# Kernel optimization log

Measured on AMD Instinct MI355X. Metric: run time of the kernel, lower is better.

The kernel has to match this reference:

```python
import jax, jax.numpy as jnp
import numpy as np

B, S, D, H, L, DFF = 32, 512, 1024, 16, 4, 2048
DK = D // H
NEG = -1e32
EPS = 1e-5


def setup_inputs() -> dict:
    key = jax.random.key(0)
    ks = jax.random.split(key, 8)
    std = 0.02
    inp = {
        "q_embed": jax.random.normal(ks[0], (B, S, D), jnp.float32),
        "qa_embed": jax.random.normal(ks[1], (B, S, D), jnp.float32),
        # per-block stacked params [L, ...]; torch Linear stored as [in, out]
        "Wk": jax.random.normal(ks[2], (L, D, D), jnp.float32) * std,
        "bk": jnp.zeros((L, D), jnp.float32),
        "Wv": jax.random.normal(ks[3], (L, D, D), jnp.float32) * std,
        "bv": jnp.zeros((L, D), jnp.float32),
        "Wo": jax.random.normal(ks[4], (L, D, D), jnp.float32) * std,
        "bo": jnp.zeros((L, D), jnp.float32),
        "ln1_s": jnp.ones((L, D), jnp.float32),
        "ln1_b": jnp.zeros((L, D), jnp.float32),
        "W1": jax.random.normal(ks[5], (L, D, DFF), jnp.float32) * std,
        "b1": jnp.zeros((L, DFF), jnp.float32),
        "W2": jax.random.normal(ks[6], (L, DFF, D), jnp.float32) * std,
        "b2": jnp.zeros((L, D), jnp.float32),
        "ln2_s": jnp.ones((L, D), jnp.float32),
        "ln2_b": jnp.zeros((L, D), jnp.float32),
    }
    return inp


def _ln(x, s, b):
    m = jnp.mean(x, axis=-1, keepdims=True)
    v = jnp.mean((x - m) ** 2, axis=-1, keepdims=True)
    return (x - m) / jnp.sqrt(v + EPS) * s + b


def _block(x, y, Wk, bk, Wv, bv, Wo, bo, l1s, l1b, W1, b1, W2, b2, l2s, l2b, allowed):
    # kq_same=1: q and k both use k_linear; q == k since query == key == x
    qk = (x @ Wk + bk).reshape(B, S, H, DK).transpose(0, 2, 1, 3)  # [B,H,S,DK]
    v = (y @ Wv + bv).reshape(B, S, H, DK).transpose(0, 2, 1, 3)
    scores = jnp.einsum("bhid,bhjd->bhij", qk, qk) / np.sqrt(DK)
    scores = jnp.where(allowed, scores, NEG)  # strictly-causal mask
    attn = jax.nn.softmax(scores, axis=-1)
    attn = attn * (jnp.arange(S)[None, None, :, None] > 0)  # zero_pad row 0
    o = jnp.einsum("bhij,bhjd->bhid", attn, v)  # [B,H,S,DK]
    o = o.transpose(0, 2, 1, 3).reshape(B, S, D) @ Wo + bo
    x = _ln(x + o, l1s, l1b)
    f = jax.nn.relu(x @ W1 + b1) @ W2 + b2
    return _ln(x + f, l2s, l2b)


def reference(q_embed, qa_embed, Wk, bk, Wv, bv, Wo, bo, ln1_s, ln1_b,
              W1, b1, W2, b2, ln2_s, ln2_b):
    allowed = jnp.tril(jnp.ones((S, S), bool), -1)  # j < i
    x, y = q_embed, qa_embed
    for i in range(L):
        x = _block(x, y, Wk[i], bk[i], Wv[i], bv[i], Wo[i], bo[i],
                   ln1_s[i], ln1_b[i], W1[i], b1[i], W2[i], b2[i],
                   ln2_s[i], ln2_b[i], allowed)
    return x
```

## Files before the change

kernel.cpp:

```cpp
#include <hip/hip_runtime.h>

#define B_ 32
#define S_ 512
#define D_ 1024
#define H_ 16
#define DK_ 64
#define DFF_ 2048
#define L_ 4

typedef __attribute__((ext_vector_type(8))) short short8;
typedef __attribute__((ext_vector_type(4))) float f32x4;
typedef unsigned short u16;
typedef unsigned int u32;
typedef __attribute__((ext_vector_type(4))) u16 u16x4;
typedef __attribute__((ext_vector_type(8))) u16 u16x8;

__device__ __forceinline__ u16 f2bf(float f) {
    u32 u = __float_as_uint(f);
    u = u + 0x7fffu + ((u >> 16) & 1u);
    return (u16)(u >> 16);
}
__device__ __forceinline__ u16 f2bf_t(float f) {
    return (u16)(__float_as_uint(f) >> 16);
}
__device__ __forceinline__ float bf2f(u16 v) {
    return __uint_as_float(((u32)v) << 16);
}

__device__ __forceinline__ void async16(const u16* g, u16* l) {
    __builtin_amdgcn_global_load_lds((const __attribute__((address_space(1))) u32*)g,
                                     (__attribute__((address_space(3))) u32*)l, 16, 0, 0);
}

#define READ_A(P)                                                              \
    afr[0][0] = *(const short8*)&lds[cb + arow + (2*(P)+0)*1024 + chv0];       \
    afr[0][1] = *(const short8*)&lds[cb + arow + (2*(P)+0)*1024 + chv1];       \
    afr[1][0] = *(const short8*)&lds[cb + arow + (2*(P)+1)*1024 + chv0];       \
    afr[1][1] = *(const short8*)&lds[cb + arow + (2*(P)+1)*1024 + chv1];

#define MFMA_PHASE(P)                                                          \
    __builtin_amdgcn_s_barrier();                                              \
    asm volatile("s_waitcnt lgkmcnt(0)" ::: "memory");                         \
    __builtin_amdgcn_sched_barrier(0);                                         \
    __builtin_amdgcn_s_setprio(1);                                             \
    _Pragma("unroll")                                                          \
    for (int mi2 = 0; mi2 < 2; mi2++) {                                        \
        _Pragma("unroll")                                                      \
        for (int ni = 0; ni < 4; ni++) {                                       \
            acc[2*(P)+mi2][ni] = __builtin_amdgcn_mfma_f32_16x16x32_bf16(      \
                afr[mi2][0], bfr[ni][0], acc[2*(P)+mi2][ni], 0, 0, 0);         \
            acc[2*(P)+mi2][ni] = __builtin_amdgcn_mfma_f32_16x16x32_bf16(      \
                afr[mi2][1], bfr[ni][1], acc[2*(P)+mi2][ni], 0, 0, 0);         \
        }                                                                      \
    }                                                                          \
    __builtin_amdgcn_s_setprio(0);

template<int RELU, int OUTM>
__global__ __launch_bounds__(512, 2)
void gemm256(const u16* __restrict__ A, const u16* __restrict__ Bt,
             const float* __restrict__ bias, void* __restrict__ C,
             int M, int N, int K)
{
    __shared__ __align__(16) u16 lds[65536];
    const int t = threadIdx.x;
    const int w = t >> 6, l = t & 63;
    const int lane16 = l & 15, quad = l >> 4;
    const int wm = w >> 2, wn = w & 3;

    const int gx = gridDim.x;
    const int nwg = gx * gridDim.y;
    const int orig = blockIdx.y * gx + blockIdx.x;
    const int q8 = nwg >> 3, r8 = nwg & 7;
    const int xcd = orig & 7, sidx = orig >> 3;
    const int nid = (xcd < r8 ? xcd * (q8 + 1) : r8 * (q8 + 1) + (xcd - r8) * q8) + sidx;
    const int m0 = (nid / gx) * 256;
    const int n0 = (nid % gx) * 256;

    f32x4 acc[8][4];
#pragma unroll
    for (int i = 0; i < 8; i++)
#pragma unroll
        for (int j = 0; j < 4; j++) acc[i][j] = f32x4{0.f, 0.f, 0.f, 0.f};

    const int lr = l >> 3;
    const int xorcol = ((l & 7) ^ lr) * 8;
    const int aw8 = (w < 4 ? w * 8 : 128 + (w - 4) * 8);
    const u16* Asrc = A + (size_t)(m0 + aw8 + lr) * K + xorcol;
    const u16* Bsrc = Bt + (size_t)(n0 + w * 8 + lr) * K + xorcol;

    auto stageA = [&](int tile, int q) {
        const int c = tile & 1;
        async16(Asrc + (size_t)(q * 32) * K + (tile << 6),
                &lds[c * 16384 + (aw8 + q * 32) * 64]);
    };
    auto stageB = [&](int tile, int j) {
        const int c = tile & 1;
        async16(Bsrc + (size_t)(j * 64) * K + (tile << 6),
                &lds[32768 + c * 16384 + (j * 64 + w * 8) * 64]);
    };

    const int chv0 = ((0 + quad) ^ (lane16 & 7)) * 8;
    const int chv1 = ((4 + quad) ^ (lane16 & 7)) * 8;
    const int arow = (wm * 128 + lane16) * 64;
    const int brow = 32768 + (wn * 64 + lane16) * 64;

    const int NT = K >> 6;

    stageA(0, 0); stageB(0, 0); stageB(0, 1);
    stageA(0, 1); stageB(0, 2); stageB(0, 3);
    stageA(0, 2);
    stageA(0, 3);
    stageA(1, 0); stageB(1, 0); stageB(1, 1);
    stageA(1, 1); stageB(1, 2); stageB(1, 3);
    stageA(1, 2);
    asm volatile("s_waitcnt vmcnt(7)" ::: "memory");
    __builtin_amdgcn_sched_barrier(0);
    __builtin_amdgcn_s_barrier();

    for (int tt = 0; tt < NT; tt++) {
        const int cb = (tt & 1) * 16384;
        short8 bfr[4][2], afr[2][2];
        if (tt + 1 < NT) stageA(tt + 1, 3);
#pragma unroll
        for (int ni = 0; ni < 4; ni++) {
            bfr[ni][0] = *(const short8*)&lds[cb + brow + ni * 1024 + chv0];
            bfr[ni][1] = *(const short8*)&lds[cb + brow + ni * 1024 + chv1];
        }
        READ_A(0)
        MFMA_PHASE(0)
        __builtin_amdgcn_s_barrier();
        if (tt + 2 < NT) { stageA(tt + 2, 0); stageB(tt + 2, 0); stageB(tt + 2, 1); }
        READ_A(1)
        MFMA_PHASE(1)
        __builtin_amdgcn_s_barrier();
        if (tt + 2 < NT) { stageA(tt + 2, 1); stageB(tt + 2, 2); stageB(tt + 2, 3); }
        READ_A(2)
        MFMA_PHASE(2)
        __builtin_amdgcn_s_barrier();
        if (tt + 2 < NT) stageA(tt + 2, 2);
        READ_A(3)
        MFMA_PHASE(3)
        if (tt + 2 < NT) asm volatile("s_waitcnt vmcnt(7)" ::: "memory");
        else             asm volatile("s_waitcnt vmcnt(0)" ::: "memory");
        __builtin_amdgcn_sched_barrier(0);
        __builtin_amdgcn_s_barrier();
    }

#pragma unroll
    for (int mi = 0; mi < 8; mi++) {
#pragma unroll
        for (int ni = 0; ni < 4; ni++) {
            int col = n0 + wn * 64 + ni * 16 + lane16;
            float bv = bias[col];
            if (OUTM == 2) {
                int tok0 = m0 + wm * 128 + mi * 16 + quad * 4;
                int bb = tok0 >> 9, s0 = tok0 & 511;
                int hh = col >> 6, dd = col & 63;
                u16x4 pk;
#pragma unroll
                for (int r2 = 0; r2 < 4; r2++) pk[r2] = f2bf(acc[mi][ni][r2] + bv);
                *(u16x4*)&((u16*)C)[(((size_t)bb * H_ + hh) * DK_ + dd) * S_ + s0] = pk;
            } else {
                int row = m0 + wm * 128 + mi * 16 + quad * 4;
#pragma unroll
                for (int r2 = 0; r2 < 4; r2++) {
                    float v = acc[mi][ni][r2] + bv;
                    if (RELU) v = fmaxf(v, 0.f);
                    size_t idx = (size_t)(row + r2) * N + col;
                    if (OUTM == 1) ((u16*)C)[idx] = f2bf(v);
                    else           ((float*)C)[idx] = v;
                }
            }
        }
    }
}

__global__ __launch_bounds__(256, 3)
void attn_kernel(const u16* __restrict__ qk, const u16* __restrict__ vt,
                 u16* __restrict__ ao)
{
    __shared__ __align__(16) u16 sP[4][32 * 72];
    const int t = threadIdx.x, w = t >> 6, l = t & 63;
    const int lane16 = l & 15, quad = l >> 4;
    const int p = blockIdx.x;
    const int bh = blockIdx.y;
    const int b = bh >> 4, h = bh & 15;
    const int band = (w < 2) ? (2 * p + w) : (15 - 2 * p - (w - 2));
    const int band0 = band * 32;
    const u16* kb = qk + (size_t)b * S_ * D_ + h * DK_;
    const u16* vb = vt + (size_t)bh * DK_ * S_;
    u16* aob = ao + (size_t)b * S_ * D_ + h * DK_;
    const float SC = 0.125f * 1.44269504f;
    u16* myP = sP[w];

    short8 bq[2][2];
#pragma unroll
    for (int ii = 0; ii < 2; ii++)
#pragma unroll
        for (int kf = 0; kf < 2; kf++)
            bq[ii][kf] = *(const short8*)(kb + (size_t)(band0 + ii * 16 + lane16) * D_ +
                                          kf * 32 + quad * 8);

    f32x4 aco[4][2];
    float lsum[2] = {0.f, 0.f};
#pragma unroll
    for (int di = 0; di < 4; di++)
#pragma unroll
        for (int ii = 0; ii < 2; ii++) aco[di][ii] = f32x4{0.f, 0.f, 0.f, 0.f};

    const int ntiles = (band >> 1) + 1;
    for (int jt = 0; jt < ntiles; jt++) {
        const int j0 = jt * 64;
        const bool diag = (jt == ntiles - 1);

        short8 aK[2][4];
#pragma unroll
        for (int kf = 0; kf < 2; kf++)
#pragma unroll
            for (int ji = 0; ji < 4; ji++)
                aK[kf][ji] = *(const short8*)(kb + (size_t)(j0 + ji * 16 + lane16) * D_ +
                                              kf * 32 + quad * 8);
        f32x4 sacc[4][2];
#pragma unroll
        for (int ji = 0; ji < 4; ji++)
#pragma unroll
            for (int ii = 0; ii < 2; ii++) sacc[ji][ii] = f32x4{0.f, 0.f, 0.f, 0.f};
#pragma unroll
        for (int kf = 0; kf < 2; kf++)
#pragma unroll
            for (int ji = 0; ji < 4; ji++)
#pragma unroll
                for (int ii = 0; ii < 2; ii++)
                    sacc[ji][ii] = __builtin_amdgcn_mfma_f32_16x16x32_bf16(
                        aK[kf][ji], bq[ii][kf], sacc[ji][ii], 0, 0, 0);

        short8 aV[2][4];
#pragma unroll
        for (int kf = 0; kf < 2; kf++)
#pragma unroll
            for (int di = 0; di < 4; di++)
                aV[kf][di] = *(const short8*)(vb + (size_t)(di * 16 + lane16) * S_ +
                                              j0 + kf * 32 + quad * 8);

#pragma unroll
        for (int ii = 0; ii < 2; ii++) {
#pragma unroll
            for (int ji = 0; ji < 4; ji++) {
                u16x4 pk;
#pragma unroll
                for (int r2 = 0; r2 < 4; r2++) {
                    float v = sacc[ji][ii][r2] * SC;
                    if (diag) {
                        int j = j0 + ji * 16 + quad * 4 + r2;
                        int i = band0 + ii * 16 + lane16;
                        if (j >= i) v = -3e38f;
                    }
                    float pv = exp2f(v);
                    lsum[ii] += pv;
                    pk[r2] = f2bf_t(pv);
                }
                *(u16x4*)&myP[(ii * 16 + lane16) * 72 + ji * 16 + quad * 4] = pk;
            }
        }

        short8 pf[2][2];
#pragma unroll
        for (int kf = 0; kf < 2; kf++)
#pragma unroll
            for (int ii = 0; ii < 2; ii++)
                pf[kf][ii] = *(const short8*)&myP[(ii * 16 + lane16) * 72 +
                                                  kf * 32 + quad * 8];
#pragma unroll
        for (int kf = 0; kf < 2; kf++)
#pragma unroll
            for (int di = 0; di < 4; di++)
#pragma unroll
                for (int ii = 0; ii < 2; ii++)
                    aco[di][ii] = __builtin_amdgcn_mfma_f32_16x16x32_bf16(
                        aV[kf][di], pf[kf][ii], aco[di][ii], 0, 0, 0);
    }

#pragma unroll
    for (int ii = 0; ii < 2; ii++) {
        lsum[ii] += __shfl_xor(lsum[ii], 16);
        lsum[ii] += __shfl_xor(lsum[ii], 32);
    }

#pragma unroll
    for (int ii = 0; ii < 2; ii++) {
        int row = band0 + ii * 16 + lane16;
        float lv = lsum[ii];
        float inv = (row == 0 || !(lv > 0.f)) ? 0.f : 1.f / lv;
#pragma unroll
        for (int di = 0; di < 4; di++) {
            u16x4 o;
#pragma unroll
            for (int r2 = 0; r2 < 4; r2++) o[r2] = f2bf(aco[di][ii][r2] * inv);
            *(u16x4*)&aob[(size_t)row * D_ + di * 16 + quad * 4] = o;
        }
    }
}

template<int XBF, int WF32>
__global__ __launch_bounds__(256)
void ln_kernel(const void* __restrict__ xin, const float* __restrict__ addv,
               const float* __restrict__ sc, const float* __restrict__ bi,
               u16* __restrict__ xb_out, float* __restrict__ f32_out)
{
    const int row = blockIdx.x;
    const int t = threadIdx.x;
    const int w = t >> 6, l = t & 63;
    __shared__ float red[8];
    f32x4 a;
    if (XBF) {
        u16x4 raw = ((const u16x4*)xin)[(size_t)row * 256 + t];
#pragma unroll
        for (int j = 0; j < 4; j++) a[j] = bf2f(raw[j]);
    } else {
        a = ((const f32x4*)xin)[(size_t)row * 256 + t];
    }
    f32x4 c = ((const f32x4*)(addv + (size_t)row * D_))[t];
    f32x4 v;
    float s1 = 0.f, s2 = 0.f;
#pragma unroll
    for (int j = 0; j < 4; j++) {
        v[j] = a[j] + c[j];
        s1 += v[j];
        s2 += v[j] * v[j];
    }
#pragma unroll
    for (int off = 32; off > 0; off >>= 1) {
        s1 += __shfl_xor(s1, off);
        s2 += __shfl_xor(s2, off);
    }
    if (l == 0) { red[w * 2] = s1; red[w * 2 + 1] = s2; }
    __syncthreads();
    s1 = red[0] + red[2] + red[4] + red[6];
    s2 = red[1] + red[3] + red[5] + red[7];
    float mean = s1 * (1.f / D_);
    float var = s2 * (1.f / D_) - mean * mean;
    float rstd = rsqrtf(var + 1e-5f);
    f32x4 s4 = ((const f32x4*)sc)[t];
    f32x4 b4 = ((const f32x4*)bi)[t];
    f32x4 o;
    u16x4 ob;
#pragma unroll
    for (int j = 0; j < 4; j++) {
        o[j] = (v[j] - mean) * rstd * s4[j] + b4[j];
        ob[j] = f2bf(o[j]);
    }
    ((u16x4*)(xb_out + (size_t)row * D_))[t] = ob;
    if (WF32) ((f32x4*)(f32_out + (size_t)row * D_))[t] = o;
}

__global__ void cvt_kernel(const float* __restrict__ in, u16* __restrict__ out, int n4)
{
    int i = blockIdx.x * blockDim.x + threadIdx.x;
    if (i < n4) {
        f32x4 v = ((const f32x4*)in)[i];
        u16x4 o;
#pragma unroll
        for (int j = 0; j < 4; j++) o[j] = f2bf(v[j]);
        ((u16x4*)out)[i] = o;
    }
}

__device__ __forceinline__ void tconv_body(const float* W, u16* WT, int K, int N,
                                           int bx, int by, int t)
{
    __shared__ float tile[64][65];
    const int n0 = bx * 64, k0 = by * 64;
#pragma unroll
    for (int i = 0; i < 4; i++) {
        int kr = (t >> 4) + i * 16;
        int nc = (t & 15) * 4;
        f32x4 v = *(const f32x4*)&W[(size_t)(k0 + kr) * N + n0 + nc];
        tile[kr][nc] = v[0]; tile[kr][nc + 1] = v[1];
        tile[kr][nc + 2] = v[2]; tile[kr][nc + 3] = v[3];
    }
    __syncthreads();
#pragma unroll
    for (int i = 0; i < 4; i++) {
        int nr = (t >> 4) + i * 16;
        int kc = (t & 15) * 4;
        u16x4 o;
#pragma unroll
        for (int j = 0; j < 4; j++) o[j] = f2bf(tile[kc + j][nr]);
        *(u16x4*)&WT[(size_t)(n0 + nr) * K + k0 + kc] = o;
    }
}

__global__ __launch_bounds__(256)
void wconv_kernel(const float* __restrict__ Wk, const float* __restrict__ Wv,
                  const float* __restrict__ Wo, const float* __restrict__ W1f,
                  const float* __restrict__ W2f,
                  u16* __restrict__ wk, u16* __restrict__ wv, u16* __restrict__ wo,
                  u16* __restrict__ w1, u16* __restrict__ w2)
{
    const int idx = blockIdx.x;
    const float* W; u16* T; int K, N, bx, by;
    if (idx < 768) {
        int wsel = idx >> 8, t16 = idx & 255;
        W = (wsel == 0) ? Wk : (wsel == 1) ? Wv : Wo;
        T = (wsel == 0) ? wk : (wsel == 1) ? wv : wo;
        K = 1024; N = 1024; bx = t16 & 15; by = t16 >> 4;
    } else if (idx < 1280) {
        int i = idx - 768;
        W = W1f; T = w1; K = 1024; N = 2048; bx = i & 31; by = i >> 5;
    } else {
        int i = idx - 1280;
        W = W2f; T = w2; K = 2048; N = 1024; bx = i & 15; by = i >> 4;
    }
    tconv_body(W, T, K, N, bx, by, threadIdx.x);
}

extern "C" void kernel_launch(void* const* d_in, const int* in_sizes, int n_in,
                              void* d_out, int out_size, void* d_ws, size_t ws_size,
                              hipStream_t stream)
{
    const float* q_embed = (const float*)d_in[0];
    const float* qa_embed = (const float*)d_in[1];
    const float* Wk = (const float*)d_in[2];
    const float* bk = (const float*)d_in[3];
    const float* Wv = (const float*)d_in[4];
    const float* bv = (const float*)d_in[5];
    const float* Wo = (const float*)d_in[6];
    const float* bo = (const float*)d_in[7];
    const float* ln1_s = (const float*)d_in[8];
    const float* ln1_b = (const float*)d_in[9];
    const float* W1 = (const float*)d_in[10];
    const float* b1 = (const float*)d_in[11];
    const float* W2 = (const float*)d_in[12];
    const float* b2 = (const float*)d_in[13];
    const float* ln2_s = (const float*)d_in[14];
    const float* ln2_b = (const float*)d_in[15];
    (void)in_sizes; (void)n_in; (void)out_size;

    char* ws = (char*)d_ws;
    size_t off = 0;
    auto carve = [&](size_t bytes) -> char* {
        char* p = ws + off;
        off += (bytes + 255) & ~(size_t)255;
        return p;
    };
    const size_t NTOK = (size_t)B_ * S_;
    u16* wk = (u16*)carve((size_t)D_ * D_ * 2);
    u16* wv = (u16*)carve((size_t)D_ * D_ * 2);
    u16* wo = (u16*)carve((size_t)D_ * D_ * 2);
    u16* w1 = (u16*)carve((size_t)D_ * DFF_ * 2);
    u16* w2 = (u16*)carve((size_t)DFF_ * D_ * 2);
    u16* x = (u16*)carve(NTOK * D_ * 2);
    u16* U12 = (u16*)carve(NTOK * DFF_ * 2);
    u16* U3 = (u16*)carve(NTOK * D_ * 2);
    size_t off_overlay = off;
    u16* ybf_sep = (u16*)carve(NTOK * D_ * 2);
    bool sep = (ws_size >= off);
    if (!sep) off = off_overlay;
    if (ws_size < off) return;

    u16* qkb = U12;
    u16* vbf = U12 + NTOK * D_;
    u16* hb = U12;
    u16* aob = U3;
    u16* ybf = sep ? ybf_sep : U3;
    float* of32 = (float*)d_out;

    cvt_kernel<<<16384, 256, 0, stream>>>(q_embed, x, (int)(NTOK * D_ / 4));
    if (sep)
        cvt_kernel<<<16384, 256, 0, stream>>>(qa_embed, ybf, (int)(NTOK * D_ / 4));

    const dim3 G1024(4, 64), G2048(8, 64);
    for (int lyr = 0; lyr < L_; lyr++) {
        const size_t wsq = (size_t)lyr * D_ * D_;
        const size_t wf1 = (size_t)lyr * D_ * DFF_;
        wconv_kernel<<<1792, 256, 0, stream>>>(Wk + wsq, Wv + wsq, Wo + wsq,
                                               W1 + wf1, W2 + wf1,
                                               wk, wv, wo, w1, w2);
        if (!sep)
            cvt_kernel<<<16384, 256, 0, stream>>>(qa_embed, ybf, (int)(NTOK * D_ / 4));
        gemm256<0, 1><<<G1024, 512, 0, stream>>>(x, wk, bk + lyr * D_,
                                                 qkb, (int)NTOK, D_, D_);
        gemm256<0, 2><<<G1024, 512, 0, stream>>>(ybf, wv, bv + lyr * D_,
                                                 vbf, (int)NTOK, D_, D_);
        attn_kernel<<<dim3(4, B_ * H_), 256, 0, stream>>>(qkb, vbf, aob);
        gemm256<0, 0><<<G1024, 512, 0, stream>>>(aob, wo, bo + lyr * D_,
                                                 of32, (int)NTOK, D_, D_);
        if (lyr == 0)
            ln_kernel<0, 0><<<(int)NTOK, 256, 0, stream>>>(q_embed, of32,
                ln1_s + lyr * D_, ln1_b + lyr * D_, x, nullptr);
        else
            ln_kernel<1, 0><<<(int)NTOK, 256, 0, stream>>>(x, of32,
                ln1_s + lyr * D_, ln1_b + lyr * D_, x, nullptr);
        gemm256<1, 1><<<G2048, 512, 0, stream>>>(x, w1, b1 + lyr * DFF_,
                                                 hb, (int)NTOK, DFF_, D_);
        gemm256<0, 0><<<G1024, 512, 0, stream>>>(hb, w2, b2 + lyr * D_,
                                                 of32, (int)NTOK, D_, DFF_);
        if (lyr == L_ - 1)
            ln_kernel<1, 1><<<(int)NTOK, 256, 0, stream>>>(x, of32,
                ln2_s + lyr * D_, ln2_b + lyr * D_, x, (float*)d_out);
        else
            ln_kernel<1, 0><<<(int)NTOK, 256, 0, stream>>>(x, of32,
                ln2_s + lyr * D_, ln2_b + lyr * D_, x, nullptr);
    }
}
```

Baseline: 1.798 ms.

## Software-pipeline LDS fragment reads against MFMAs in GEMM main loop

Restructures the GEMM K-loop into eight MFMA phases, each split by k-half. The A/B fragment reads for the next phase are issued from LDS while the current phase's MFMAs run, with partial lgkmcnt waits instead of full drains. The next tile's first fragments are prefetched across the iteration boundary, and the global-to-LDS staging order is rebalanced to interleave A and B loads. The aim is to hide LDS latency behind MFMA work. In exchange there are more barriers per tile and more register pressure, and the hand-tuned waitcnt counts must match the exact read order to stay correct.

```diff
diff --git a/kernel.cpp b/kernel.cpp
--- a/kernel.cpp
+++ b/kernel.cpp
@@ -32,28 +32,29 @@
                                      (__attribute__((address_space(3))) u32*)l, 16, 0, 0);
 }
 
-#define READ_A(P)                                                              \
-    afr[0][0] = *(const short8*)&lds[cb + arow + (2*(P)+0)*1024 + chv0];       \
-    afr[0][1] = *(const short8*)&lds[cb + arow + (2*(P)+0)*1024 + chv1];       \
-    afr[1][0] = *(const short8*)&lds[cb + arow + (2*(P)+1)*1024 + chv0];       \
-    afr[1][1] = *(const short8*)&lds[cb + arow + (2*(P)+1)*1024 + chv1];
-
-#define MFMA_PHASE(P)                                                          \
-    __builtin_amdgcn_s_barrier();                                              \
-    asm volatile("s_waitcnt lgkmcnt(0)" ::: "memory");                         \
+#define RD_A2(dst, CBX, MP, CHV)                                               \
+    dst[0] = *(const short8*)&lds[(CBX) + arow + (2*(MP)+0)*1024 + (CHV)];     \
+    dst[1] = *(const short8*)&lds[(CBX) + arow + (2*(MP)+1)*1024 + (CHV)];
+
+#define RD_B4(dst, CBX, CHV)                                                   \
+    _Pragma("unroll")                                                          \
+    for (int ni = 0; ni < 4; ni++)                                             \
+        dst[ni] = *(const short8*)&lds[32768 + (CBX) + browr + ni*1024 + (CHV)];
+
+#define MF8(MP, ASRC, BSRC, LGN)                                               \
+    asm volatile("s_waitcnt lgkmcnt(" #LGN ")" ::: "memory");                  \
     __builtin_amdgcn_sched_barrier(0);                                         \
     __builtin_amdgcn_s_setprio(1);                                             \
     _Pragma("unroll")                                                          \
-    for (int mi2 = 0; mi2 < 2; mi2++) {                                        \
-        _Pragma("unroll")                                                      \
-        for (int ni = 0; ni < 4; ni++) {                                       \
-            acc[2*(P)+mi2][ni] = __builtin_amdgcn_mfma_f32_16x16x32_bf16(      \
-                afr[mi2][0], bfr[ni][0], acc[2*(P)+mi2][ni], 0, 0, 0);         \
-            acc[2*(P)+mi2][ni] = __builtin_amdgcn_mfma_f32_16x16x32_bf16(      \
-                afr[mi2][1], bfr[ni][1], acc[2*(P)+mi2][ni], 0, 0, 0);         \
-        }                                                                      \
+    for (int ni = 0; ni < 4; ni++) {                                           \
+        acc[2*(MP)+0][ni] = __builtin_amdgcn_mfma_f32_16x16x32_bf16(           \
+            ASRC[0], BSRC[ni], acc[2*(MP)+0][ni], 0, 0, 0);                    \
+        acc[2*(MP)+1][ni] = __builtin_amdgcn_mfma_f32_16x16x32_bf16(           \
+            ASRC[1], BSRC[ni], acc[2*(MP)+1][ni], 0, 0, 0);                    \
     }                                                                          \
-    __builtin_amdgcn_s_setprio(0);
+    __builtin_amdgcn_s_setprio(0);                                             \
+    __builtin_amdgcn_s_barrier();                                              \
+    __builtin_amdgcn_sched_barrier(0);
 
 template<int RELU, int OUTM>
 __global__ __launch_bounds__(512, 2)
@@ -101,49 +102,63 @@
 
     const int chv0 = ((0 + quad) ^ (lane16 & 7)) * 8;
     const int chv1 = ((4 + quad) ^ (lane16 & 7)) * 8;
-    const int arow = (wm * 128 + lane16) * 64;
-    const int brow = 32768 + (wn * 64 + lane16) * 64;
+    const int arow  = (wm * 128 + lane16) * 64;
+    const int browr = (wn * 64 + lane16) * 64;
 
     const int NT = K >> 6;
 
-    stageA(0, 0); stageB(0, 0); stageB(0, 1);
-    stageA(0, 1); stageB(0, 2); stageB(0, 3);
-    stageA(0, 2);
-    stageA(0, 3);
-    stageA(1, 0); stageB(1, 0); stageB(1, 1);
-    stageA(1, 1); stageB(1, 2); stageB(1, 3);
-    stageA(1, 2);
-    asm volatile("s_waitcnt vmcnt(7)" ::: "memory");
+    stageA(0, 0); stageB(0, 0); stageA(0, 1); stageB(0, 1);
+    stageA(0, 2); stageB(0, 2); stageA(0, 3); stageB(0, 3);
+    stageA(1, 0); stageB(1, 0); stageA(1, 1); stageB(1, 1);
+    stageA(1, 2); stageB(1, 2);
+    asm volatile("s_waitcnt vmcnt(6)" ::: "memory");
     __builtin_amdgcn_sched_barrier(0);
     __builtin_amdgcn_s_barrier();
 
+    short8 a0[2], a1[2], bk0[4], bk1[4];
+    RD_B4(bk0, 0, chv0)
+    RD_A2(a0, 0, 0, chv0)
+
     for (int tt = 0; tt < NT; tt++) {
-        const int cb = (tt & 1) * 16384;
-        short8 bfr[4][2], afr[2][2];
-        if (tt + 1 < NT) stageA(tt + 1, 3);
-#pragma unroll
-        for (int ni = 0; ni < 4; ni++) {
-            bfr[ni][0] = *(const short8*)&lds[cb + brow + ni * 1024 + chv0];
-            bfr[ni][1] = *(const short8*)&lds[cb + brow + ni * 1024 + chv1];
-        }
-        READ_A(0)
-        MFMA_PHASE(0)
-        __builtin_amdgcn_s_barrier();
-        if (tt + 2 < NT) { stageA(tt + 2, 0); stageB(tt + 2, 0); stageB(tt + 2, 1); }
-        READ_A(1)
-        MFMA_PHASE(1)
-        __builtin_amdgcn_s_barrier();
-        if (tt + 2 < NT) { stageA(tt + 2, 1); stageB(tt + 2, 2); stageB(tt + 2, 3); }
-        READ_A(2)
-        MFMA_PHASE(2)
-        __builtin_amdgcn_s_barrier();
-        if (tt + 2 < NT) stageA(tt + 2, 2);
-        READ_A(3)
-        MFMA_PHASE(3)
-        if (tt + 2 < NT) asm volatile("s_waitcnt vmcnt(7)" ::: "memory");
-        else             asm volatile("s_waitcnt vmcnt(0)" ::: "memory");
+        const int cb  = (tt & 1) << 14;
+        const int cbn = ((tt + 1) & 1) << 14;
+        const bool hn1 = (tt + 1 < NT);
+        const bool hn2 = (tt + 2 < NT);
+
+        RD_A2(a1, cb, 1, chv0)
+        MF8(0, a0, bk0, 2)
+        if (hn1) { stageA(tt + 1, 3); stageB(tt + 1, 3); }
+        RD_A2(a0, cb, 2, chv0)
+        bk1[0] = *(const short8*)&lds[32768 + cb + browr + 0 * 1024 + chv1];
+        bk1[1] = *(const short8*)&lds[32768 + cb + browr + 1 * 1024 + chv1];
+        MF8(1, a1, bk0, 4)
+        RD_A2(a1, cb, 3, chv0)
+        bk1[2] = *(const short8*)&lds[32768 + cb + browr + 2 * 1024 + chv1];
+        bk1[3] = *(const short8*)&lds[32768 + cb + browr + 3 * 1024 + chv1];
+        MF8(2, a0, bk0, 6)
+        RD_A2(a0, cb, 0, chv1)
+        MF8(3, a1, bk0, 4)
+        RD_A2(a1, cb, 1, chv1)
+        MF8(0, a0, bk1, 2)
+        if (hn2) { stageA(tt + 2, 0); stageB(tt + 2, 0); }
+        RD_A2(a0, cb, 2, chv1)
+        MF8(1, a1, bk1, 2)
+        if (hn2) { stageA(tt + 2, 1); stageB(tt + 2, 1); }
+        RD_A2(a1, cb, 3, chv1)
+        MF8(2, a0, bk1, 2)
+        if (hn2) { stageA(tt + 2, 2); stageB(tt + 2, 2); }
+        if (hn2) asm volatile("s_waitcnt vmcnt(6)" ::: "memory");
+        else     asm volatile("s_waitcnt vmcnt(0)" ::: "memory");
         __builtin_amdgcn_sched_barrier(0);
         __builtin_amdgcn_s_barrier();
+        __builtin_amdgcn_sched_barrier(0);
+        if (hn1) {
+            RD_B4(bk0, cbn, chv0)
+            RD_A2(a0, cbn, 0, chv0)
+            MF8(3, a1, bk1, 6)
+        } else {
+            MF8(3, a1, bk1, 0)
+        }
     }
 
 #pragma unroll
```

New measurement: 1.793 ms. About the same (-0.3%).

## Restructure GEMM main loop into quadrant MFMA phases with 2x unrolled double-buffer

Applied to the files above, without the earlier changes.

Replaces the four row-phase MFMA schedule with a quadrant schedule: each wave loads a 4-row A quarter and a 2-column B half, so fragments are reused across two MFMA quadrants. The loop is unrolled by two K tiles so buffer offsets are compile-time constants. Global-to-LDS staging is interleaved between the quadrant phases with explicit barriers and waitcnts. The goal is to reduce LDS read traffic per MFMA and overlap loads with compute better. The cost is more barriers per tile and a tighter dependency on exact waitcnt counts.

```diff
diff --git a/kernel.cpp b/kernel.cpp
--- a/kernel.cpp
+++ b/kernel.cpp
@@ -32,28 +32,38 @@
                                      (__attribute__((address_space(3))) u32*)l, 16, 0, 0);
 }
 
-#define READ_A(P)                                                              \
-    afr[0][0] = *(const short8*)&lds[cb + arow + (2*(P)+0)*1024 + chv0];       \
-    afr[0][1] = *(const short8*)&lds[cb + arow + (2*(P)+0)*1024 + chv1];       \
-    afr[1][0] = *(const short8*)&lds[cb + arow + (2*(P)+1)*1024 + chv0];       \
-    afr[1][1] = *(const short8*)&lds[cb + arow + (2*(P)+1)*1024 + chv1];
-
-#define MFMA_PHASE(P)                                                          \
-    __builtin_amdgcn_s_barrier();                                              \
+#define LGKM0_FENCE                                                            \
     asm volatile("s_waitcnt lgkmcnt(0)" ::: "memory");                         \
-    __builtin_amdgcn_sched_barrier(0);                                         \
+    __builtin_amdgcn_sched_barrier(0);
+
+#define MFQ(MQ, NQ, BQ)                                                        \
     __builtin_amdgcn_s_setprio(1);                                             \
     _Pragma("unroll")                                                          \
-    for (int mi2 = 0; mi2 < 2; mi2++) {                                        \
+    for (int r = 0; r < 4; r++) {                                              \
         _Pragma("unroll")                                                      \
-        for (int ni = 0; ni < 4; ni++) {                                       \
-            acc[2*(P)+mi2][ni] = __builtin_amdgcn_mfma_f32_16x16x32_bf16(      \
-                afr[mi2][0], bfr[ni][0], acc[2*(P)+mi2][ni], 0, 0, 0);         \
-            acc[2*(P)+mi2][ni] = __builtin_amdgcn_mfma_f32_16x16x32_bf16(      \
-                afr[mi2][1], bfr[ni][1], acc[2*(P)+mi2][ni], 0, 0, 0);         \
+        for (int c = 0; c < 2; c++) {                                          \
+            _Pragma("unroll")                                                  \
+            for (int kf = 0; kf < 2; kf++)                                     \
+                acc[(MQ)*4+r][(NQ)*2+c] =                                      \
+                    __builtin_amdgcn_mfma_f32_16x16x32_bf16(                   \
+                        a[r][kf], BQ[c][kf], acc[(MQ)*4+r][(NQ)*2+c], 0,0,0);  \
         }                                                                      \
     }                                                                          \
     __builtin_amdgcn_s_setprio(0);
+
+#define RD_AQ(CBA, MQ)                                                         \
+    _Pragma("unroll")                                                          \
+    for (int r = 0; r < 4; r++) {                                              \
+        a[r][0] = *(const short8*)&lds[(CBA) + arow + (MQ)*4096 + r*1024 + chv0]; \
+        a[r][1] = *(const short8*)&lds[(CBA) + arow + (MQ)*4096 + r*1024 + chv1]; \
+    }
+
+#define RD_BQ(DST, CBB, NQ)                                                    \
+    _Pragma("unroll")                                                          \
+    for (int c = 0; c < 2; c++) {                                              \
+        DST[c][0] = *(const short8*)&lds[(CBB) + brow + (NQ)*2048 + c*1024 + chv0]; \
+        DST[c][1] = *(const short8*)&lds[(CBB) + brow + (NQ)*2048 + c*1024 + chv1]; \
+    }
 
 template<int RELU, int OUTM>
 __global__ __launch_bounds__(512, 2)
@@ -102,46 +112,76 @@
     const int chv0 = ((0 + quad) ^ (lane16 & 7)) * 8;
     const int chv1 = ((4 + quad) ^ (lane16 & 7)) * 8;
     const int arow = (wm * 128 + lane16) * 64;
-    const int brow = 32768 + (wn * 64 + lane16) * 64;
+    const int brow = (wn * 64 + lane16) * 64;
 
     const int NT = K >> 6;
-
-    stageA(0, 0); stageB(0, 0); stageB(0, 1);
-    stageA(0, 1); stageB(0, 2); stageB(0, 3);
-    stageA(0, 2);
-    stageA(0, 3);
-    stageA(1, 0); stageB(1, 0); stageB(1, 1);
-    stageA(1, 1); stageB(1, 2); stageB(1, 3);
-    stageA(1, 2);
-    asm volatile("s_waitcnt vmcnt(7)" ::: "memory");
+    const int niter = NT >> 1;
+
+    stageA(0, 0); stageA(0, 1); stageA(0, 2); stageA(0, 3);
+    stageB(0, 0); stageB(0, 1); stageB(0, 2); stageB(0, 3);
+    stageA(1, 0); stageA(1, 1);
+    stageB(1, 0); stageB(1, 1); stageB(1, 2); stageB(1, 3);
+    stageA(1, 2); stageA(1, 3);
+    asm volatile("s_waitcnt vmcnt(8)" ::: "memory");
     __builtin_amdgcn_sched_barrier(0);
     __builtin_amdgcn_s_barrier();
 
-    for (int tt = 0; tt < NT; tt++) {
-        const int cb = (tt & 1) * 16384;
-        short8 bfr[4][2], afr[2][2];
-        if (tt + 1 < NT) stageA(tt + 1, 3);
-#pragma unroll
-        for (int ni = 0; ni < 4; ni++) {
-            bfr[ni][0] = *(const short8*)&lds[cb + brow + ni * 1024 + chv0];
-            bfr[ni][1] = *(const short8*)&lds[cb + brow + ni * 1024 + chv1];
-        }
-        READ_A(0)
-        MFMA_PHASE(0)
-        __builtin_amdgcn_s_barrier();
-        if (tt + 2 < NT) { stageA(tt + 2, 0); stageB(tt + 2, 0); stageB(tt + 2, 1); }
-        READ_A(1)
-        MFMA_PHASE(1)
-        __builtin_amdgcn_s_barrier();
-        if (tt + 2 < NT) { stageA(tt + 2, 1); stageB(tt + 2, 2); stageB(tt + 2, 3); }
-        READ_A(2)
-        MFMA_PHASE(2)
-        __builtin_amdgcn_s_barrier();
-        if (tt + 2 < NT) stageA(tt + 2, 2);
-        READ_A(3)
-        MFMA_PHASE(3)
-        if (tt + 2 < NT) asm volatile("s_waitcnt vmcnt(7)" ::: "memory");
-        else             asm volatile("s_waitcnt vmcnt(0)" ::: "memory");
+    short8 a[4][2], b0[2][2], b1[2][2];
+
+    for (int it = 0; it < niter; it++) {
+        const bool hn = (it + 1 < niter);
+        const int e2 = 2 * it + 2, o2 = 2 * it + 3;
+
+        RD_AQ(0, 0)
+        RD_BQ(b0, 32768, 0)
+        asm volatile("s_waitcnt lgkmcnt(8)" ::: "memory");
+        __builtin_amdgcn_s_barrier();
+        LGKM0_FENCE
+        MFQ(0, 0, b0)
+        __builtin_amdgcn_s_barrier();
+        RD_BQ(b1, 32768, 1)
+        if (hn) { stageA(e2, 0); stageA(e2, 1); }
+        __builtin_amdgcn_s_barrier();
+        LGKM0_FENCE
+        MFQ(0, 1, b1)
+        __builtin_amdgcn_s_barrier();
+        RD_AQ(0, 1)
+        if (hn) { stageB(e2, 0); stageB(e2, 1); }
+        __builtin_amdgcn_s_barrier();
+        LGKM0_FENCE
+        MFQ(1, 0, b0)
+        __builtin_amdgcn_s_barrier();
+        if (hn) { stageB(e2, 2); stageB(e2, 3); stageA(e2, 2); stageA(e2, 3); }
+        __builtin_amdgcn_s_barrier();
+        MFQ(1, 1, b1)
+        if (hn) asm volatile("s_waitcnt vmcnt(8)" ::: "memory");
+        else    asm volatile("s_waitcnt vmcnt(0)" ::: "memory");
+        __builtin_amdgcn_sched_barrier(0);
+        __builtin_amdgcn_s_barrier();
+
+        RD_AQ(16384, 0)
+        RD_BQ(b0, 49152, 0)
+        asm volatile("s_waitcnt lgkmcnt(8)" ::: "memory");
+        __builtin_amdgcn_s_barrier();
+        LGKM0_FENCE
+        MFQ(0, 0, b0)
+        __builtin_amdgcn_s_barrier();
+        RD_BQ(b1, 49152, 1)
+        if (hn) { stageA(o2, 0); stageA(o2, 1); }
+        __builtin_amdgcn_s_barrier();
+        LGKM0_FENCE
+        MFQ(0, 1, b1)
+        __builtin_amdgcn_s_barrier();
+        RD_AQ(16384, 1)
+        if (hn) { stageB(o2, 0); stageB(o2, 1); }
+        __builtin_amdgcn_s_barrier();
+        LGKM0_FENCE
+        MFQ(1, 0, b0)
+        __builtin_amdgcn_s_barrier();
+        if (hn) { stageB(o2, 2); stageB(o2, 3); stageA(o2, 2); stageA(o2, 3); }
+        __builtin_amdgcn_s_barrier();
+        MFQ(1, 1, b1)
+        if (hn) asm volatile("s_waitcnt vmcnt(8)" ::: "memory");
         __builtin_amdgcn_sched_barrier(0);
         __builtin_amdgcn_s_barrier();
     }
```

After: 1.759 ms. -2.2%, faster.
